# Kernel tuning notes

Measured on AMD Instinct MI355X. Metric: run time of the kernel, lower is better.

## Reference

```python
import jax, jax.numpy as jnp
import numpy as np

LN_EPS = 1e-5
NORM_EPS = 1e-12
SLOPE = 0.1

def _layernorm(x, g, b):
    m = jnp.mean(x, axis=-1, keepdims=True)
    v = jnp.mean(jnp.square(x - m), axis=-1, keepdims=True)
    return (x - m) * jax.lax.rsqrt(v + LN_EPS) * g + b

def _leaky(x):
    return jnp.where(x >= 0, x, SLOPE * x)

def setup_inputs() -> dict:
    key = jax.random.key(0)
    ks = jax.random.split(key, 8)
    N = 1048576
    features = jax.random.normal(ks[0], (N, 128), dtype=jnp.float32)
    # PyTorch Linear default init: U(-1/sqrt(fan_in), 1/sqrt(fan_in))
    W1 = jax.random.uniform(ks[1], (32, 128), jnp.float32, -1/np.sqrt(128), 1/np.sqrt(128))
    g1 = jnp.ones((32,), jnp.float32); b1 = jnp.zeros((32,), jnp.float32)
    W2 = jax.random.uniform(ks[2], (16, 32), jnp.float32, -1/np.sqrt(32), 1/np.sqrt(32))
    g2 = jnp.ones((16,), jnp.float32); b2 = jnp.zeros((16,), jnp.float32)
    W3 = jax.random.uniform(ks[3], (3, 16), jnp.float32, -1/np.sqrt(16), 1/np.sqrt(16))
    b3 = jax.random.uniform(ks[4], (3,), jnp.float32, -1/np.sqrt(16), 1/np.sqrt(16))
    return {"features": features, "W1": W1, "g1": g1, "b1": b1,
            "W2": W2, "g2": g2, "b2": b2, "W3": W3, "b3": b3}

def reference(features, W1, g1, b1, W2, g2, b2, W3, b3):
    x = features @ W1.T                       # [N,32]
    x = _leaky(_layernorm(x, g1, b1))
    x = x @ W2.T                               # [N,16]
    x = _leaky(_layernorm(x, g2, b2))
    x = x @ W3.T + b3                          # [N,3]
    # F.normalize(dim=-1): x / max(||x||_2, eps)
    n = jnp.linalg.norm(x, axis=-1, keepdims=True)
    return x / jnp.maximum(n, NORM_EPS)
```

## Files before the change

kernel.cpp:

```cpp
#include <hip/hip_runtime.h>
#include <math.h>

typedef short bf16x8 __attribute__((ext_vector_type(8)));
typedef float f32x4  __attribute__((ext_vector_type(4)));

#define TPB 256
#define ROWS 256
#define CSTRIDE 36
#define BFR_BYTES 16384
#define PK(lo, hi) (((lo) >> 16) | ((hi) & 0xffff0000u))
#define BOFF(nt, ks, p) ((((nt)*4 + (ks))*2 + (p))*256)

__device__ __forceinline__ void split2A(float x, unsigned &h1, unsigned &h2) {
    unsigned u = __float_as_uint(x);
    h1 = (u + 0x7fffu + ((u >> 16) & 1u)) & 0xffff0000u;
    h2 = __float_as_uint(x - __uint_as_float(h1));
}
__device__ __forceinline__ void split2W(float x, unsigned &h1, unsigned &h2) {
    unsigned u = __float_as_uint(x);
    h1 = (u + 0x7fffu + ((u >> 16) & 1u)) & 0xffff0000u;
    float r1 = x - __uint_as_float(h1);
    unsigned u1 = __float_as_uint(r1);
    h2 = (u1 + 0x7fffu + ((u1 >> 16) & 1u)) & 0xffff0000u;
}

__global__ __launch_bounds__(TPB, 3) void decoder_kernel(
    const float* __restrict__ feat,
    const float* __restrict__ W1, const float* __restrict__ g1, const float* __restrict__ b1,
    const float* __restrict__ W2, const float* __restrict__ g2, const float* __restrict__ b2,
    const float* __restrict__ W3, const float* __restrict__ b3,
    float* __restrict__ out, int N)
{
    __shared__ __align__(16) unsigned char lds[BFR_BYTES + ROWS * CSTRIDE * 4];
    unsigned* bfr = (unsigned*)lds;
    float*    Ct  = (float*)(lds + BFR_BYTES);

    const int t = threadIdx.x;
    const int l = t & 63;
    const int w = t >> 6;
    const size_t blk0 = (size_t)blockIdx.x * ROWS;

    for (int c = t; c < 512; c += 256) {
        const int lc = c & 63, ks = (c >> 6) & 3, nt = (c >> 8) & 1;
        const float* wp = W1 + (nt * 16 + (lc & 15)) * 128 + ks * 32 + (lc >> 4) * 8;
        float v[8];
        *(float4*)(v)     = *(const float4*)(wp);
        *(float4*)(v + 4) = *(const float4*)(wp + 4);
        unsigned h1[8], h2[8];
#pragma unroll
        for (int i = 0; i < 8; ++i) split2W(v[i], h1[i], h2[i]);
        uint4 q1 = {PK(h1[0],h1[1]), PK(h1[2],h1[3]), PK(h1[4],h1[5]), PK(h1[6],h1[7])};
        uint4 q2 = {PK(h2[0],h2[1]), PK(h2[2],h2[3]), PK(h2[4],h2[5]), PK(h2[6],h2[7])};
        *(uint4*)(bfr + BOFF(nt, ks, 0) + lc * 4) = q1;
        *(uint4*)(bfr + BOFF(nt, ks, 1) + lc * 4) = q2;
    }
    __syncthreads();

    const int arow = l & 15;
    const int acol = (l >> 4) * 8;
    float4 buf[2][8];
    {
        size_t rr = blk0 + (size_t)w * 64 + arow;
        if (rr >= (size_t)N) rr = N - 1;
        const float* ap = feat + rr * 128 + acol;
#pragma unroll
        for (int ks = 0; ks < 4; ++ks) {
            buf[0][2 * ks]     = *(const float4*)(ap + ks * 32);
            buf[0][2 * ks + 1] = *(const float4*)(ap + ks * 32 + 4);
        }
    }

#pragma unroll
    for (int j = 0; j < 4; ++j) {
        if (j < 3) {
            size_t rr = blk0 + (size_t)w * 64 + (j + 1) * 16 + arow;
            if (rr >= (size_t)N) rr = N - 1;
            const float* ap = feat + rr * 128 + acol;
#pragma unroll
            for (int ks = 0; ks < 4; ++ks) {
                buf[(j + 1) & 1][2 * ks]     = *(const float4*)(ap + ks * 32);
                buf[(j + 1) & 1][2 * ks + 1] = *(const float4*)(ap + ks * 32 + 4);
            }
        }
        f32x4 acc0 = {0.f, 0.f, 0.f, 0.f};
        f32x4 acc1 = {0.f, 0.f, 0.f, 0.f};
#pragma unroll
        for (int ks = 0; ks < 4; ++ks) {
            float v[8];
            *(float4*)(v)     = buf[j & 1][2 * ks];
            *(float4*)(v + 4) = buf[j & 1][2 * ks + 1];
            unsigned h1[8], h2[8];
#pragma unroll
            for (int i = 0; i < 8; ++i) split2A(v[i], h1[i], h2[i]);
            uint4 q1 = {PK(h1[0],h1[1]), PK(h1[2],h1[3]), PK(h1[4],h1[5]), PK(h1[6],h1[7])};
            uint4 q2 = {PK(h2[0],h2[1]), PK(h2[2],h2[3]), PK(h2[4],h2[5]), PK(h2[6],h2[7])};
            bf16x8 a1 = __builtin_bit_cast(bf16x8, q1);
            bf16x8 a2 = __builtin_bit_cast(bf16x8, q2);
            bf16x8 B10 = __builtin_bit_cast(bf16x8, *(const uint4*)(bfr + BOFF(0, ks, 0) + l * 4));
            bf16x8 B20 = __builtin_bit_cast(bf16x8, *(const uint4*)(bfr + BOFF(0, ks, 1) + l * 4));
            bf16x8 B11 = __builtin_bit_cast(bf16x8, *(const uint4*)(bfr + BOFF(1, ks, 0) + l * 4));
            bf16x8 B21 = __builtin_bit_cast(bf16x8, *(const uint4*)(bfr + BOFF(1, ks, 1) + l * 4));
            acc0 = __builtin_amdgcn_mfma_f32_16x16x32_bf16(a1, B10, acc0, 0, 0, 0);
            acc1 = __builtin_amdgcn_mfma_f32_16x16x32_bf16(a1, B11, acc1, 0, 0, 0);
            acc0 = __builtin_amdgcn_mfma_f32_16x16x32_bf16(a2, B10, acc0, 0, 0, 0);
            acc1 = __builtin_amdgcn_mfma_f32_16x16x32_bf16(a2, B11, acc1, 0, 0, 0);
            acc0 = __builtin_amdgcn_mfma_f32_16x16x32_bf16(a1, B20, acc0, 0, 0, 0);
            acc1 = __builtin_amdgcn_mfma_f32_16x16x32_bf16(a1, B21, acc1, 0, 0, 0);
        }
        const int crow = w * 64 + j * 16 + (l >> 4) * 4;
        const int ccol = l & 15;
#pragma unroll
        for (int r = 0; r < 4; ++r) {
            Ct[(crow + r) * CSTRIDE + ccol]      = acc0[r];
            Ct[(crow + r) * CSTRIDE + 16 + ccol] = acc1[r];
        }
    }
    __syncthreads();

    float x[32];
#pragma unroll
    for (int c = 0; c < 8; ++c)
        *(float4*)(x + c * 4) = *(const float4*)(Ct + t * CSTRIDE + c * 4);

    float m = 0.f;
#pragma unroll
    for (int j = 0; j < 32; ++j) m += x[j];
    m *= (1.f / 32.f);
    float var = 0.f;
#pragma unroll
    for (int j = 0; j < 32; ++j) { const float d = x[j] - m; var = fmaf(d, d, var); }
    var *= (1.f / 32.f);
    const float rs1 = rsqrtf(var + 1e-5f);

    float z[32];
#pragma unroll
    for (int j = 0; j < 32; ++j) {
        float y = (x[j] - m) * rs1 * g1[j] + b1[j];
        z[j] = (y >= 0.f) ? y : 0.1f * y;
    }

    float a2v[16];
#pragma unroll
    for (int k = 0; k < 16; ++k) {
        const float* __restrict__ wrow = W2 + k * 32;
        float s = 0.f;
#pragma unroll
        for (int j = 0; j < 32; ++j) s = fmaf(z[j], wrow[j], s);
        a2v[k] = s;
    }

    float m2 = 0.f;
#pragma unroll
    for (int k = 0; k < 16; ++k) m2 += a2v[k];
    m2 *= (1.f / 16.f);
    float v2 = 0.f;
#pragma unroll
    for (int k = 0; k < 16; ++k) { const float d = a2v[k] - m2; v2 = fmaf(d, d, v2); }
    v2 *= (1.f / 16.f);
    const float rs2 = rsqrtf(v2 + 1e-5f);

    float z2[16];
#pragma unroll
    for (int k = 0; k < 16; ++k) {
        float y = (a2v[k] - m2) * rs2 * g2[k] + b2[k];
        z2[k] = (y >= 0.f) ? y : 0.1f * y;
    }

    float o[3];
#pragma unroll
    for (int q = 0; q < 3; ++q) {
        const float* __restrict__ wrow = W3 + q * 16;
        float s = b3[q];
#pragma unroll
        for (int k = 0; k < 16; ++k) s = fmaf(z2[k], wrow[k], s);
        o[q] = s;
    }
    const float nrm = sqrtf(o[0]*o[0] + o[1]*o[1] + o[2]*o[2]);
    const float inv = 1.f / fmaxf(nrm, 1e-12f);

    __syncthreads();
    Ct[t * 3 + 0] = o[0] * inv;
    Ct[t * 3 + 1] = o[1] * inv;
    Ct[t * 3 + 2] = o[2] * inv;
    __syncthreads();
    const size_t ob = blk0 * 3;
    const size_t lim = (size_t)N * 3;
#pragma unroll
    for (int i = 0; i < 3; ++i) {
        const size_t gi = ob + t + i * 256;
        if (gi < lim) out[gi] = Ct[t + i * 256];
    }
}

extern "C" void kernel_launch(void* const* d_in, const int* in_sizes, int n_in,
                              void* d_out, int out_size, void* d_ws, size_t ws_size,
                              hipStream_t stream) {
    const float* feat = (const float*)d_in[0];
    const float* W1   = (const float*)d_in[1];
    const float* g1   = (const float*)d_in[2];
    const float* b1   = (const float*)d_in[3];
    const float* W2   = (const float*)d_in[4];
    const float* g2   = (const float*)d_in[5];
    const float* b2   = (const float*)d_in[6];
    const float* W3   = (const float*)d_in[7];
    const float* b3   = (const float*)d_in[8];
    float* out = (float*)d_out;

    const int N = in_sizes[0] / 128;
    const int grid = (N + ROWS - 1) / ROWS;

    decoder_kernel<<<grid, TPB, 0, stream>>>(feat, W1, g1, b1, W2, g2, b2, W3, b3, out, N);
}
```

Measured before the change: 132.4 us.

## Make decoder kernel persistent with atomic chunk scheduling and cross-chunk prefetch

```diff
diff --git a/kernel.cpp b/kernel.cpp
--- a/kernel.cpp
+++ b/kernel.cpp
@@ -8,8 +8,13 @@
 #define ROWS 256
 #define CSTRIDE 36
 #define BFR_BYTES 16384
+#define CT_BYTES (ROWS * CSTRIDE * 4)
 #define PK(lo, hi) (((lo) >> 16) | ((hi) & 0xffff0000u))
 #define BOFF(nt, ks, p) ((((nt)*4 + (ks))*2 + (p))*256)
+#define GRID 768
+
+#define WBAR() do { asm volatile("s_waitcnt lgkmcnt(0)" ::: "memory"); \
+                    __builtin_amdgcn_s_barrier(); } while (0)
 
 __device__ __forceinline__ void split2A(float x, unsigned &h1, unsigned &h2) {
     unsigned u = __float_as_uint(x);
@@ -29,16 +34,19 @@
     const float* __restrict__ W1, const float* __restrict__ g1, const float* __restrict__ b1,
     const float* __restrict__ W2, const float* __restrict__ g2, const float* __restrict__ b2,
     const float* __restrict__ W3, const float* __restrict__ b3,
-    float* __restrict__ out, int N)
+    float* __restrict__ out, int N,
+    unsigned* __restrict__ ctr, unsigned nchunks)
 {
-    __shared__ __align__(16) unsigned char lds[BFR_BYTES + ROWS * CSTRIDE * 4];
+    __shared__ __align__(16) unsigned char lds[BFR_BYTES + CT_BYTES + 16];
     unsigned* bfr = (unsigned*)lds;
     float*    Ct  = (float*)(lds + BFR_BYTES);
+    volatile unsigned* nxt_sh = (volatile unsigned*)(lds + BFR_BYTES + CT_BYTES);
 
     const int t = threadIdx.x;
     const int l = t & 63;
     const int w = t >> 6;
-    const size_t blk0 = (size_t)blockIdx.x * ROWS;
+    const int arow = l & 15;
+    const int acol = (l >> 4) * 8;
 
     for (int c = t; c < 512; c += 256) {
         const int lc = c & 63, ks = (c >> 6) & 3, nt = (c >> 8) & 1;
@@ -54,13 +62,13 @@
         *(uint4*)(bfr + BOFF(nt, ks, 0) + lc * 4) = q1;
         *(uint4*)(bfr + BOFF(nt, ks, 1) + lc * 4) = q2;
     }
+    if (t == 0) *nxt_sh = atomicAdd(ctr, 1u);
     __syncthreads();
-
-    const int arow = l & 15;
-    const int acol = (l >> 4) * 8;
+    unsigned cur = *nxt_sh;
+
     float4 buf[2][8];
-    {
-        size_t rr = blk0 + (size_t)w * 64 + arow;
+    if (cur < nchunks) {
+        size_t rr = (size_t)cur * ROWS + (size_t)w * 64 + arow;
         if (rr >= (size_t)N) rr = N - 1;
         const float* ap = feat + rr * 128 + acol;
 #pragma unroll
@@ -70,125 +78,139 @@
         }
     }
 
-#pragma unroll
-    for (int j = 0; j < 4; ++j) {
-        if (j < 3) {
-            size_t rr = blk0 + (size_t)w * 64 + (j + 1) * 16 + arow;
+    while (cur < nchunks) {
+        const size_t blk0 = (size_t)cur * ROWS;
+
+#pragma unroll
+        for (int j = 0; j < 4; ++j) {
+            if (j == 1 && t == 0) *nxt_sh = atomicAdd(ctr, 1u);
+            if (j < 3) {
+                size_t rr = blk0 + (size_t)w * 64 + (j + 1) * 16 + arow;
+                if (rr >= (size_t)N) rr = N - 1;
+                const float* ap = feat + rr * 128 + acol;
+#pragma unroll
+                for (int ks = 0; ks < 4; ++ks) {
+                    buf[(j + 1) & 1][2 * ks]     = *(const float4*)(ap + ks * 32);
+                    buf[(j + 1) & 1][2 * ks + 1] = *(const float4*)(ap + ks * 32 + 4);
+                }
+            }
+            f32x4 acc0 = {0.f, 0.f, 0.f, 0.f};
+            f32x4 acc1 = {0.f, 0.f, 0.f, 0.f};
+#pragma unroll
+            for (int ks = 0; ks < 4; ++ks) {
+                float v[8];
+                *(float4*)(v)     = buf[j & 1][2 * ks];
+                *(float4*)(v + 4) = buf[j & 1][2 * ks + 1];
+                unsigned h1[8], h2[8];
+#pragma unroll
+                for (int i = 0; i < 8; ++i) split2A(v[i], h1[i], h2[i]);
+                uint4 q1 = {PK(h1[0],h1[1]), PK(h1[2],h1[3]), PK(h1[4],h1[5]), PK(h1[6],h1[7])};
+                uint4 q2 = {PK(h2[0],h2[1]), PK(h2[2],h2[3]), PK(h2[4],h2[5]), PK(h2[6],h2[7])};
+                bf16x8 a1 = __builtin_bit_cast(bf16x8, q1);
+                bf16x8 a2 = __builtin_bit_cast(bf16x8, q2);
+                bf16x8 B10 = __builtin_bit_cast(bf16x8, *(const uint4*)(bfr + BOFF(0, ks, 0) + l * 4));
+                bf16x8 B20 = __builtin_bit_cast(bf16x8, *(const uint4*)(bfr + BOFF(0, ks, 1) + l * 4));
+                bf16x8 B11 = __builtin_bit_cast(bf16x8, *(const uint4*)(bfr + BOFF(1, ks, 0) + l * 4));
+                bf16x8 B21 = __builtin_bit_cast(bf16x8, *(const uint4*)(bfr + BOFF(1, ks, 1) + l * 4));
+                acc0 = __builtin_amdgcn_mfma_f32_16x16x32_bf16(a1, B10, acc0, 0, 0, 0);
+                acc1 = __builtin_amdgcn_mfma_f32_16x16x32_bf16(a1, B11, acc1, 0, 0, 0);
+                acc0 = __builtin_amdgcn_mfma_f32_16x16x32_bf16(a2, B10, acc0, 0, 0, 0);
+                acc1 = __builtin_amdgcn_mfma_f32_16x16x32_bf16(a2, B11, acc1, 0, 0, 0);
+                acc0 = __builtin_amdgcn_mfma_f32_16x16x32_bf16(a1, B20, acc0, 0, 0, 0);
+                acc1 = __builtin_amdgcn_mfma_f32_16x16x32_bf16(a1, B21, acc1, 0, 0, 0);
+            }
+            const int crow = w * 64 + j * 16 + (l >> 4) * 4;
+            const int ccol = l & 15;
+#pragma unroll
+            for (int r = 0; r < 4; ++r) {
+                Ct[(crow + r) * CSTRIDE + ccol]      = acc0[r];
+                Ct[(crow + r) * CSTRIDE + 16 + ccol] = acc1[r];
+            }
+        }
+        WBAR();
+
+        float x[32];
+#pragma unroll
+        for (int c = 0; c < 8; ++c)
+            *(float4*)(x + c * 4) = *(const float4*)(Ct + t * CSTRIDE + c * 4);
+        const unsigned nxt = *nxt_sh;
+        WBAR();
+
+        if (nxt < nchunks) {
+            size_t rr = (size_t)nxt * ROWS + (size_t)w * 64 + arow;
             if (rr >= (size_t)N) rr = N - 1;
             const float* ap = feat + rr * 128 + acol;
 #pragma unroll
             for (int ks = 0; ks < 4; ++ks) {
-                buf[(j + 1) & 1][2 * ks]     = *(const float4*)(ap + ks * 32);
-                buf[(j + 1) & 1][2 * ks + 1] = *(const float4*)(ap + ks * 32 + 4);
-            }
-        }
-        f32x4 acc0 = {0.f, 0.f, 0.f, 0.f};
-        f32x4 acc1 = {0.f, 0.f, 0.f, 0.f};
-#pragma unroll
-        for (int ks = 0; ks < 4; ++ks) {
-            float v[8];
-            *(float4*)(v)     = buf[j & 1][2 * ks];
-            *(float4*)(v + 4) = buf[j & 1][2 * ks + 1];
-            unsigned h1[8], h2[8];
-#pragma unroll
-            for (int i = 0; i < 8; ++i) split2A(v[i], h1[i], h2[i]);
-            uint4 q1 = {PK(h1[0],h1[1]), PK(h1[2],h1[3]), PK(h1[4],h1[5]), PK(h1[6],h1[7])};
-            uint4 q2 = {PK(h2[0],h2[1]), PK(h2[2],h2[3]), PK(h2[4],h2[5]), PK(h2[6],h2[7])};
-            bf16x8 a1 = __builtin_bit_cast(bf16x8, q1);
-            bf16x8 a2 = __builtin_bit_cast(bf16x8, q2);
-            bf16x8 B10 = __builtin_bit_cast(bf16x8, *(const uint4*)(bfr + BOFF(0, ks, 0) + l * 4));
-            bf16x8 B20 = __builtin_bit_cast(bf16x8, *(const uint4*)(bfr + BOFF(0, ks, 1) + l * 4));
-            bf16x8 B11 = __builtin_bit_cast(bf16x8, *(const uint4*)(bfr + BOFF(1, ks, 0) + l * 4));
-            bf16x8 B21 = __builtin_bit_cast(bf16x8, *(const uint4*)(bfr + BOFF(1, ks, 1) + l * 4));
-            acc0 = __builtin_amdgcn_mfma_f32_16x16x32_bf16(a1, B10, acc0, 0, 0, 0);
-            acc1 = __builtin_amdgcn_mfma_f32_16x16x32_bf16(a1, B11, acc1, 0, 0, 0);
-            acc0 = __builtin_amdgcn_mfma_f32_16x16x32_bf16(a2, B10, acc0, 0, 0, 0);
-            acc1 = __builtin_amdgcn_mfma_f32_16x16x32_bf16(a2, B11, acc1, 0, 0, 0);
-            acc0 = __builtin_amdgcn_mfma_f32_16x16x32_bf16(a1, B20, acc0, 0, 0, 0);
-            acc1 = __builtin_amdgcn_mfma_f32_16x16x32_bf16(a1, B21, acc1, 0, 0, 0);
-        }
-        const int crow = w * 64 + j * 16 + (l >> 4) * 4;
-        const int ccol = l & 15;
-#pragma unroll
-        for (int r = 0; r < 4; ++r) {
-            Ct[(crow + r) * CSTRIDE + ccol]      = acc0[r];
-            Ct[(crow + r) * CSTRIDE + 16 + ccol] = acc1[r];
-        }
-    }
-    __syncthreads();
-
-    float x[32];
-#pragma unroll
-    for (int c = 0; c < 8; ++c)
-        *(float4*)(x + c * 4) = *(const float4*)(Ct + t * CSTRIDE + c * 4);
-
-    float m = 0.f;
-#pragma unroll
-    for (int j = 0; j < 32; ++j) m += x[j];
-    m *= (1.f / 32.f);
-    float var = 0.f;
-#pragma unroll
-    for (int j = 0; j < 32; ++j) { const float d = x[j] - m; var = fmaf(d, d, var); }
-    var *= (1.f / 32.f);
-    const float rs1 = rsqrtf(var + 1e-5f);
-
-    float z[32];
-#pragma unroll
-    for (int j = 0; j < 32; ++j) {
-        float y = (x[j] - m) * rs1 * g1[j] + b1[j];
-        z[j] = (y >= 0.f) ? y : 0.1f * y;
-    }
-
-    float a2v[16];
-#pragma unroll
-    for (int k = 0; k < 16; ++k) {
-        const float* __restrict__ wrow = W2 + k * 32;
-        float s = 0.f;
-#pragma unroll
-        for (int j = 0; j < 32; ++j) s = fmaf(z[j], wrow[j], s);
-        a2v[k] = s;
-    }
-
-    float m2 = 0.f;
-#pragma unroll
-    for (int k = 0; k < 16; ++k) m2 += a2v[k];
-    m2 *= (1.f / 16.f);
-    float v2 = 0.f;
-#pragma unroll
-    for (int k = 0; k < 16; ++k) { const float d = a2v[k] - m2; v2 = fmaf(d, d, v2); }
-    v2 *= (1.f / 16.f);
-    const float rs2 = rsqrtf(v2 + 1e-5f);
-
-    float z2[16];
-#pragma unroll
-    for (int k = 0; k < 16; ++k) {
-        float y = (a2v[k] - m2) * rs2 * g2[k] + b2[k];
-        z2[k] = (y >= 0.f) ? y : 0.1f * y;
-    }
-
-    float o[3];
-#pragma unroll
-    for (int q = 0; q < 3; ++q) {
-        const float* __restrict__ wrow = W3 + q * 16;
-        float s = b3[q];
-#pragma unroll
-        for (int k = 0; k < 16; ++k) s = fmaf(z2[k], wrow[k], s);
-        o[q] = s;
-    }
-    const float nrm = sqrtf(o[0]*o[0] + o[1]*o[1] + o[2]*o[2]);
-    const float inv = 1.f / fmaxf(nrm, 1e-12f);
-
-    __syncthreads();
-    Ct[t * 3 + 0] = o[0] * inv;
-    Ct[t * 3 + 1] = o[1] * inv;
-    Ct[t * 3 + 2] = o[2] * inv;
-    __syncthreads();
-    const size_t ob = blk0 * 3;
-    const size_t lim = (size_t)N * 3;
-#pragma unroll
-    for (int i = 0; i < 3; ++i) {
-        const size_t gi = ob + t + i * 256;
-        if (gi < lim) out[gi] = Ct[t + i * 256];
+                buf[0][2 * ks]     = *(const float4*)(ap + ks * 32);
+                buf[0][2 * ks + 1] = *(const float4*)(ap + ks * 32 + 4);
+            }
+        }
+
+        float m = 0.f;
+#pragma unroll
+        for (int j = 0; j < 32; ++j) m += x[j];
+        m *= (1.f / 32.f);
+        float var = 0.f;
+#pragma unroll
+        for (int j = 0; j < 32; ++j) { const float d = x[j] - m; var = fmaf(d, d, var); }
+        var *= (1.f / 32.f);
+        const float rs1 = rsqrtf(var + 1e-5f);
+
+        float z[32];
+#pragma unroll
+        for (int j = 0; j < 32; ++j) {
+            float y = (x[j] - m) * rs1 * g1[j] + b1[j];
+            z[j] = (y >= 0.f) ? y : 0.1f * y;
+        }
+
+        float a2v[16];
+#pragma unroll
+        for (int k = 0; k < 16; ++k) {
+            const float* __restrict__ wrow = W2 + k * 32;
+            float s = 0.f;
+#pragma unroll
+            for (int j = 0; j < 32; ++j) s = fmaf(z[j], wrow[j], s);
+            a2v[k] = s;
+        }
+
+        float m2 = 0.f;
+#pragma unroll
+        for (int k = 0; k < 16; ++k) m2 += a2v[k];
+        m2 *= (1.f / 16.f);
+        float v2 = 0.f;
+#pragma unroll
+        for (int k = 0; k < 16; ++k) { const float d = a2v[k] - m2; v2 = fmaf(d, d, v2); }
+        v2 *= (1.f / 16.f);
+        const float rs2 = rsqrtf(v2 + 1e-5f);
+
+        float z2[16];
+#pragma unroll
+        for (int k = 0; k < 16; ++k) {
+            float y = (a2v[k] - m2) * rs2 * g2[k] + b2[k];
+            z2[k] = (y >= 0.f) ? y : 0.1f * y;
+        }
+
+        float o[3];
+#pragma unroll
+        for (int q = 0; q < 3; ++q) {
+            const float* __restrict__ wrow = W3 + q * 16;
+            float s = b3[q];
+#pragma unroll
+            for (int k = 0; k < 16; ++k) s = fmaf(z2[k], wrow[k], s);
+            o[q] = s;
+        }
+        const float nrm = sqrtf(o[0]*o[0] + o[1]*o[1] + o[2]*o[2]);
+        const float inv = 1.f / fmaxf(nrm, 1e-12f);
+
+        const size_t myrow = blk0 + t;
+        if (myrow < (size_t)N) {
+            out[myrow * 3 + 0] = o[0] * inv;
+            out[myrow * 3 + 1] = o[1] * inv;
+            out[myrow * 3 + 2] = o[2] * inv;
+        }
+
+        cur = nxt;
     }
 }
 
@@ -207,7 +229,10 @@
     float* out = (float*)d_out;
 
     const int N = in_sizes[0] / 128;
-    const int grid = (N + ROWS - 1) / ROWS;
-
-    decoder_kernel<<<grid, TPB, 0, stream>>>(feat, W1, g1, b1, W2, g2, b2, W3, b3, out, N);
-}
+    const unsigned nchunks = (unsigned)((N + ROWS - 1) / ROWS);
+    unsigned* ctr = (unsigned*)d_ws;
+
+    hipMemsetAsync(ctr, 0, sizeof(unsigned), stream);
+    decoder_kernel<<<GRID, TPB, 0, stream>>>(feat, W1, g1, b1, W2, g2, b2, W3, b3,
+                                             out, N, ctr, nchunks);
+}
```

Result: faster. 126.5 us (-4.4%).
